# Optimization experiments

Hardware: AMD Instinct MI355X
Metric: run time of the kernel (lower is better)

## Reference

```python
import jax, jax.numpy as jnp
import numpy as np

N_CLASS, N_SUPPORT, N_QUERY = 5, 5, 15
C, T, V = 128, 8, 25
LN_EPS = 1e-12


def setup_inputs() -> dict:
    key = jax.random.key(0)
    ks = jax.random.split(key, 6)
    n_tot = N_CLASS * (N_SUPPORT + N_QUERY)
    inp = jax.random.normal(ks[0], (n_tot, C, T, V), dtype=jnp.float32)
    # episode labels: 20 consecutive samples per class (arange // per_class)
    target = (jnp.arange(n_tot, dtype=jnp.int32) // (N_SUPPORT + N_QUERY)).astype(jnp.int32)
    s = 0.02
    p = lambda k: jax.random.normal(k, (C, C), dtype=jnp.float32) * s
    return {
        'input': inp,
        'Wq': p(ks[1]), 'bq': jnp.zeros((C,), jnp.float32),
        'Wk': p(ks[2]), 'bk': jnp.zeros((C,), jnp.float32),
        'Wv': p(ks[3]), 'bv': jnp.zeros((C,), jnp.float32),
        'Wo': p(ks[4]), 'bo': jnp.zeros((C,), jnp.float32),
        'ln_g': jnp.ones((C,), jnp.float32), 'ln_b': jnp.zeros((C,), jnp.float32),
        'target': target,
        'n_support': N_SUPPORT,
    }


def _layer_norm(x, g, b):
    mu = x.mean(-1, keepdims=True)
    var = ((x - mu) ** 2).mean(-1, keepdims=True)
    return (x - mu) * jax.lax.rsqrt(var + LN_EPS) * g + b


def _episode_forward(input, Wq, bq, Wk, bk, Wv, bv, Wo, bo, ln_g, ln_b, target, n_support):
    n_tot, c, t, v = input.shape
    m = N_CLASS
    per_class = n_tot // m
    n_query = per_class - n_support
    n = m * n_query

    # support/query split (stable argsort == torch.where per class for sorted labels)
    order = jnp.argsort(target).reshape(m, per_class)
    supp_idx = order[:, :n_support]                      # (m, h)
    qry_idx = order[:, n_support:].reshape(-1)           # (n,)
    z_proto = input[supp_idx]                            # (m, h, c, t, v)
    zq = input[qry_idx]                                  # (n, c, t, v)

    # ---- hal(): pairwise cross-attention over the vertex axis ----
    mh = m * n_support
    zq_p = jnp.transpose(zq, (0, 2, 3, 1))                                   # (n, t, v, c)
    zp_p = jnp.transpose(z_proto.reshape(mh, c, t, v), (0, 2, 3, 1))          # (mh, t, v, c)
    cat = jnp.concatenate([zq_p, zp_p], axis=0)                               # (n1, t, v, c)
    n1 = cat.shape[0]

    # Q from each of the n1 items, K/V from each of the mh prototypes.
    # Equivalent to the original expand->reshape pairing, without duplicating K/V.
    Q = cat @ Wq + bq                                                         # (n1, t, v, c)
    K = zp_p @ Wk + bk                                                        # (mh, t, v, c)
    Vv = zp_p @ Wv + bv                                                       # (mh, t, v, c)
    scale = 1.0 / jnp.sqrt(jnp.asarray(c, dtype=Q.dtype))
    scores = jnp.einsum('ntqc,mtkc->nmtqk', Q, K) * scale                     # (n1, mh, t, v, v)
    attn = jax.nn.softmax(scores, axis=-1)
    ctx = jnp.einsum('nmtqk,mtkc->nmtqc', attn, Vv)                           # (n1, mh, t, v, c)
    out = _layer_norm(ctx @ Wo + bo + cat[:, None], ln_g, ln_b)               # residual + LN
    att = out.mean(axis=1)                                                    # (n1, t, v, c) mean over mh pairs

    zq_att = jnp.transpose(att[:n], (0, 3, 1, 2))                             # (n, c, t, v)
    proto_att = att[n:].reshape(m, n_support, t, v, c).mean(axis=1)           # (m, t, v, c)
    proto_att = jnp.transpose(proto_att, (0, 3, 1, 2))                        # (m, c, t, v)

    # ---- squared-Euclidean metric on flattened features ----
    zq_f = zq_att.reshape(n, -1)
    zp_f = proto_att.reshape(m, -1)
    dist = jnp.sum((zq_f[:, None, :] - zp_f[None, :, :]) ** 2, axis=-1)       # (n, m)

    log_p_y = jax.nn.log_softmax(-dist, axis=1).reshape(m, n_query, m)
    cls = jnp.arange(m)
    loss = -log_p_y[cls[:, None], jnp.arange(n_query)[None, :], cls[:, None]].mean()
    y_hat = jnp.argmax(log_p_y, axis=2)
    acc = (y_hat == cls[:, None]).astype(jnp.float32).mean()
    return loss, acc


def reference(input, Wq, bq, Wk, bk, Wv, bv, Wo, bo, ln_g, ln_b, target, n_support):
    return _episode_forward(input, Wq, bq, Wk, bk, Wv, bv, Wo, bo, ln_g, ln_b, target, n_support)
```

## Files before the change

kernel.cpp:

```cpp
#include <hip/hip_runtime.h>
#include <math.h>

#define NTOT 100
#define NQ   75
#define NP   25
#define CC   128
#define TT   8
#define VV   25
#define NCLS 5
#define NSUP 5
#define NQRY 15
#define ROW  (TT*VV*CC)
#define TILE (VV*CC)
#define ROWS_Q 20000
#define ROWS_S 5000
#define RB_Q 625
#define RB_S 157

typedef __attribute__((ext_vector_type(8))) short short8;
typedef __attribute__((ext_vector_type(16))) float f32x16;

typedef union { uint4 u4; short8 s8; } pk_t;

__device__ __forceinline__ ushort f2bf(float f) {
    uint u = __float_as_uint(f);
    u += 0x7FFFu + ((u >> 16) & 1u);
    return (ushort)(u >> 16);
}
__device__ __forceinline__ float bf2f(uint u16v) {
    return __uint_as_float(u16v << 16);
}
__device__ __forceinline__ uint pkbf(float a, float b) {
    return (uint)f2bf(a) | ((uint)f2bf(b) << 16);
}

__global__ __launch_bounds__(256) void k_prep(
    const float* __restrict__ input, const int* __restrict__ target,
    const float* __restrict__ Wq, const float* __restrict__ Wk,
    const float* __restrict__ Wv, const float* __restrict__ Wo,
    ushort* __restrict__ catQbf, ushort* __restrict__ catSbf,
    ushort* __restrict__ Wfrag, ushort* __restrict__ catC,
    int* __restrict__ counter) {
    __shared__ float smp[100 * 129];
    __shared__ int targ[NTOT];
    __shared__ int order[NTOT];
    int b = blockIdx.x, tid = threadIdx.x;

    if (b < 200) {
        int n = b >> 1, hf = b & 1;
        if (tid < NTOT) targ[tid] = target[tid];
        __syncthreads();
        if (tid < NTOT) {
            int ti = targ[tid], rank = 0;
            for (int j = 0; j < NTOT; ++j) {
                int tj = targ[j];
                rank += (tj < ti) || (tj == ti && j < tid);
            }
            order[rank] = tid;
        }
        __syncthreads();
        int src;
        if (n < NQ) { int m = n / NQRY, qq = n - m * NQRY; src = order[m * 20 + NSUP + qq]; }
        else        { int i = n - NQ; int m = i / NSUP, s = i - m * NSUP; src = order[m * 20 + s]; }

        const float* in = input + (size_t)src * ROW + hf * 100;
        for (int idx = tid; idx < 12800; idx += 256) {
            int c = idx / 100, tt = idx - c * 100;
            smp[tt * 129 + c] = in[c * 200 + tt];
        }
        __syncthreads();
        uint* cc = (uint*)catC + ((size_t)n * 200 + hf * 100) * 64;
        for (int e2 = tid; e2 < 6400; e2 += 256) {
            int r = e2 >> 6, c2 = e2 & 63;
            cc[r * 64 + c2] = pkbf(smp[r * 129 + c2 * 2], smp[r * 129 + c2 * 2 + 1]);
        }
        bool isSup = (n >= NQ);
        for (int o = tid; o < 1600; o += 256) {
            int k8 = o / 100, tt = o - k8 * 100;
            int base = tt * 129 + k8 * 8;
            uint4 pk;
            pk.x = pkbf(smp[base+0], smp[base+1]);
            pk.y = pkbf(smp[base+2], smp[base+3]);
            pk.z = pkbf(smp[base+4], smp[base+5]);
            pk.w = pkbf(smp[base+6], smp[base+7]);
            int row = n * 200 + hf * 100 + tt;
            size_t dst = (((size_t)(row >> 5) * 8 + (k8 >> 1)) * 64 + ((row & 31) + 32 * (k8 & 1))) * 8;
            *(uint4*)(catQbf + dst) = pk;
            if (isSup) {
                int r2 = (n - NQ) * 200 + hf * 100 + tt;
                size_t dst2 = (((size_t)(r2 >> 5) * 8 + (k8 >> 1)) * 64 + ((r2 & 31) + 32 * (k8 & 1))) * 8;
                *(uint4*)(catSbf + dst2) = pk;
            }
        }
    } else {
        int wi = b - 200;
        const float* W = (wi == 0) ? Wq : (wi == 1) ? Wk : (wi == 2) ? Wv : Wo;
        ushort* dstW = Wfrag + (size_t)wi * 16384;
        for (int o = tid; o < 2048; o += 256) {
            int k8 = o >> 7, c = o & 127;
            uint4 pk;
            pk.x = pkbf(W[(k8*8+0)*128 + c], W[(k8*8+1)*128 + c]);
            pk.y = pkbf(W[(k8*8+2)*128 + c], W[(k8*8+3)*128 + c]);
            pk.z = pkbf(W[(k8*8+4)*128 + c], W[(k8*8+5)*128 + c]);
            pk.w = pkbf(W[(k8*8+6)*128 + c], W[(k8*8+7)*128 + c]);
            size_t dst = ((size_t)((c >> 5) * 8 + (k8 >> 1)) * 64 + ((c & 31) + 32 * (k8 & 1))) * 8;
            *(uint4*)(dstW + dst) = pk;
        }
        if (wi == 3) {
            uint4 z = make_uint4(0, 0, 0, 0);
            for (int o = tid; o < 512; o += 256) {
                int ks = o >> 6, l = o & 63;
                if ((l & 31) >= 8)
                    *(uint4*)(catSbf + (((size_t)156 * 8 + ks) * 64 + l) * 8) = z;
            }
            if (tid == 0) *counter = 0;
        }
    }
}

__global__ __launch_bounds__(256) void k_proj(
    const ushort* __restrict__ catQbf, const ushort* __restrict__ catSbf,
    const ushort* __restrict__ Wfrag, const float* __restrict__ bq,
    const float* __restrict__ bk, const float* __restrict__ bv,
    ushort* __restrict__ Qf, ushort* __restrict__ Kf, ushort* __restrict__ Vf) {
    __shared__ ushort Vt[128 * 136];
    int b = blockIdx.x, tid = threadIdx.x;
    int w = tid >> 6, lane = tid & 63;
    int typ, rb0, nrb;
    if (b < 157)      { typ = 0; rb0 = b * 4;         nrb = RB_Q; }
    else if (b < 197) { typ = 1; rb0 = (b - 157) * 4; nrb = RB_S; }
    else              { typ = 2; rb0 = (b - 197) * 4; nrb = RB_S; }
    int rowblk = rb0 + w;
    bool act = rowblk < nrb;
    const ushort* src = (typ == 0) ? catQbf : catSbf;
    const ushort* Wf = Wfrag + (size_t)typ * 16384;
    const float* bias = (typ == 0) ? bq : (typ == 1) ? bk : bv;
    int rlimit = (typ == 0) ? ROWS_Q : ROWS_S;

    short8 af[8];
    if (act) {
        const ushort* ap = src + (size_t)rowblk * 4096 + lane * 8;
        #pragma unroll
        for (int ks = 0; ks < 8; ++ks) af[ks] = *(const short8*)(ap + ks * 512);
    }
    #pragma unroll
    for (int ct = 0; ct < 4; ++ct) {
        f32x16 Cm;
        #pragma unroll
        for (int r = 0; r < 16; ++r) Cm[r] = 0.f;
        if (act) {
            const ushort* bp = Wf + (size_t)(ct * 8) * 512 + lane * 8;
            #pragma unroll
            for (int ks = 0; ks < 8; ++ks) {
                short8 bf_ = *(const short8*)(bp + ks * 512);
                Cm = __builtin_amdgcn_mfma_f32_32x32x16_bf16(af[ks], bf_, Cm, 0, 0, 0);
            }
            float bcol = bias[ct * 32 + (lane & 31)];
            if (typ <= 1) {
                ushort* dstB = (typ == 0) ? Qf : Kf;
                #pragma unroll
                for (int r = 0; r < 16; ++r) {
                    int row = rowblk * 32 + (r & 3) + 8 * (r >> 2) + 4 * (lane >> 5);
                    if (row < rlimit) {
                        int c = ct * 32 + (lane & 31);
                        int st = row / 25, vv = row - st * 25;
                        size_t dst = (((size_t)st * 8 + (c >> 4)) * 64 + (vv + 32 * ((c >> 3) & 1))) * 8 + (c & 7);
                        dstB[dst] = f2bf(Cm[r] + bcol);
                    }
                }
            } else {
                #pragma unroll
                for (int r = 0; r < 16; ++r) {
                    int lrow = w * 32 + (r & 3) + 8 * (r >> 2) + 4 * (lane >> 5);
                    Vt[lrow * 136 + ct * 32 + (lane & 31)] = f2bf(Cm[r] + bcol);
                }
            }
        }
    }
    if (typ == 2) {
        __syncthreads();
        const ushort* WoF = Wfrag + (size_t)3 * 16384;
        short8 a2[8];
        if (act) {
            #pragma unroll
            for (int ks = 0; ks < 8; ++ks)
                a2[ks] = *(const short8*)(Vt + (w * 32 + (lane & 31)) * 136 + ks * 16 + (lane >> 5) * 8);
        }
        #pragma unroll
        for (int ct = 0; ct < 4; ++ct) {
            if (act) {
                f32x16 Cm;
                #pragma unroll
                for (int r = 0; r < 16; ++r) Cm[r] = 0.f;
                const ushort* bp = WoF + (size_t)(ct * 8) * 512 + lane * 8;
                #pragma unroll
                for (int ks = 0; ks < 8; ++ks) {
                    short8 bf_ = *(const short8*)(bp + ks * 512);
                    Cm = __builtin_amdgcn_mfma_f32_32x32x16_bf16(a2[ks], bf_, Cm, 0, 0, 0);
                }
                #pragma unroll
                for (int r = 0; r < 16; ++r) {
                    int row = rowblk * 32 + (r & 3) + 8 * (r >> 2) + 4 * (lane >> 5);
                    if (row < ROWS_S) {
                        int c = ct * 32 + (lane & 31);
                        int tile = row / 25, vv = row - tile * 25;
                        size_t dst = ((((size_t)tile * 4 + ct) * 2 + (vv >> 4)) * 64
                                      + ((c & 31) + 32 * ((vv & 15) >> 3))) * 8 + (vv & 7);
                        Vf[dst] = f2bf(Cm[r]);
                    }
                }
            }
        }
    }
}

__global__ __launch_bounds__(256, 2) void k_attn(
    const ushort* __restrict__ Qf, const ushort* __restrict__ Kf,
    const ushort* __restrict__ Vf, const ushort* __restrict__ catC,
    const float* __restrict__ bo, float* __restrict__ att) {
    __shared__ float catb[25 * 129];
    __shared__ float red[2][50][65];
    __shared__ ushort qls[4096];

    int pair = blockIdx.x;
    int t = pair & 7;
    int tid = threadIdx.x;
    int wv = tid >> 6, lane = tid & 63;
    int q = lane & 31, half = lane >> 5;

    {
        const uint* cc = (const uint*)catC + (size_t)pair * 1600;
        for (int i2 = tid; i2 < 1600; i2 += 256) {
            uint u = cc[i2];
            int r = i2 >> 6, c2 = (i2 & 63) * 2;
            catb[r * 129 + c2]     = bf2f(u & 0xffffu) + bo[c2];
            catb[r * 129 + c2 + 1] = bf2f(u >> 16) + bo[c2 + 1];
        }
    }
    {
        const uint* qp = (const uint*)(Qf + (size_t)pair * 4096);
        uint* ql = (uint*)qls;
        for (int i2 = tid; i2 < 2048; i2 += 256) ql[i2] = qp[i2];
    }
    __syncthreads();

    int qc = q < 25 ? q : 24;
    float attsum[64];
    #pragma unroll
    for (int i = 0; i < 64; ++i) attsum[i] = 0.f;
    float Csc = 0.f;

    const float CEXP = (float)(1.4426950408889634 * 0.08838834764831845);

    const ushort* kbase = Kf + (size_t)t * 4096 + lane * 8;
    short8 kf[8];
    #pragma unroll
    for (int ks = 0; ks < 8; ++ks)
        kf[ks] = *(const short8*)(kbase + (size_t)wv * 32768 + ks * 512);

    int cnt = (wv == 0) ? 7 : 6;
    for (int mi = 0; mi < cnt; ++mi) {
        int m = wv + 4 * mi;

        f32x16 S;
        #pragma unroll
        for (int r = 0; r < 16; ++r) S[r] = 0.f;
        #pragma unroll
        for (int ks = 0; ks < 8; ++ks) {
            short8 qv = *(const short8*)(qls + ks * 512 + lane * 8);
            S = __builtin_amdgcn_mfma_f32_32x32x16_bf16(kf[ks], qv, S, 0, 0, 0);
        }

        float p[16], mx = -3e38f;
        #pragma unroll
        for (int r = 0; r < 16; ++r) {
            int key = (r & 3) + 8 * (r >> 2) + 4 * half;
            float v = (key < 25) ? S[r] : -3e38f;
            p[r] = v; mx = fmaxf(mx, v);
        }
        mx = fmaxf(mx, __shfl_xor(mx, 32));
        float sum = 0.f;
        #pragma unroll
        for (int r = 0; r < 16; ++r) { p[r] = exp2f((p[r] - mx) * CEXP); sum += p[r]; }
        sum += __shfl_xor(sum, 32);
        float inv = 1.f / sum;

        const ushort* vp = Vf + ((size_t)(m * 8 + t)) * 4096 + lane * 8;
        short8 vf0 = *(const short8*)(vp);
        short8 vf1 = *(const short8*)(vp + 512);
        short8 vf2 = *(const short8*)(vp + 1024);
        short8 vf3 = *(const short8*)(vp + 1536);
        short8 vf4 = *(const short8*)(vp + 2048);
        short8 vf5 = *(const short8*)(vp + 2560);
        short8 vf6 = *(const short8*)(vp + 3072);
        short8 vf7 = *(const short8*)(vp + 3584);
        #pragma unroll
        for (int ks = 0; ks < 8; ++ks)
            kf[ks] = *(const short8*)(kbase + (size_t)(m + 4) * 32768 + ks * 512);

        uint o01   = pkbf(p[0] * inv,  p[1] * inv);
        uint o23   = pkbf(p[2] * inv,  p[3] * inv);
        uint o45   = pkbf(p[4] * inv,  p[5] * inv);
        uint o67   = pkbf(p[6] * inv,  p[7] * inv);
        uint o89   = pkbf(p[8] * inv,  p[9] * inv);
        uint o1011 = pkbf(p[10] * inv, p[11] * inv);
        uint o1213 = pkbf(p[12] * inv, p[13] * inv);
        uint o1415 = pkbf(p[14] * inv, p[15] * inv);
        bool h0 = (half == 0);
        uint rA = __shfl_xor(h0 ? o45 : o01, 32);
        uint rB = __shfl_xor(h0 ? o67 : o23, 32);
        uint rC = __shfl_xor(h0 ? o1213 : o89, 32);
        uint rD = __shfl_xor(h0 ? o1415 : o1011, 32);
        pk_t P0, P1;
        P0.u4 = h0 ? make_uint4(o01, o23, rA, rB) : make_uint4(rA, rB, o45, o67);
        P1.u4 = h0 ? make_uint4(o89, o1011, rC, rD) : make_uint4(rC, rD, o1213, o1415);
        short8 pb0 = P0.s8, pb1 = P1.s8;

        f32x16 ctx[4];
        #pragma unroll
        for (int mt = 0; mt < 4; ++mt) {
            #pragma unroll
            for (int r = 0; r < 16; ++r) ctx[mt][r] = 0.f;
        }
        ctx[0] = __builtin_amdgcn_mfma_f32_32x32x16_bf16(vf0, pb0, ctx[0], 0, 0, 0);
        ctx[0] = __builtin_amdgcn_mfma_f32_32x32x16_bf16(vf1, pb1, ctx[0], 0, 0, 0);
        ctx[1] = __builtin_amdgcn_mfma_f32_32x32x16_bf16(vf2, pb0, ctx[1], 0, 0, 0);
        ctx[1] = __builtin_amdgcn_mfma_f32_32x32x16_bf16(vf3, pb1, ctx[1], 0, 0, 0);
        ctx[2] = __builtin_amdgcn_mfma_f32_32x32x16_bf16(vf4, pb0, ctx[2], 0, 0, 0);
        ctx[2] = __builtin_amdgcn_mfma_f32_32x32x16_bf16(vf5, pb1, ctx[2], 0, 0, 0);
        ctx[3] = __builtin_amdgcn_mfma_f32_32x32x16_bf16(vf6, pb0, ctx[3], 0, 0, 0);
        ctx[3] = __builtin_amdgcn_mfma_f32_32x32x16_bf16(vf7, pb1, ctx[3], 0, 0, 0);

        float s1 = 0.f, s2 = 0.f;
        #pragma unroll
        for (int mt = 0; mt < 4; ++mt) {
            float t1 = 0.f, t2 = 0.f;
            #pragma unroll
            for (int r = 0; r < 16; ++r) {
                int c = mt * 32 + (r & 3) + 8 * (r >> 2) + 4 * half;
                float xv = ctx[mt][r] + catb[qc * 129 + c];
                ctx[mt][r] = xv;
                t1 += xv; t2 = fmaf(xv, xv, t2);
            }
            s1 += t1; s2 += t2;
        }
        s1 += __shfl_xor(s1, 32); s2 += __shfl_xor(s2, 32);
        float mu = s1 * (1.f / 128.f);
        float var = s2 * (1.f / 128.f) - mu * mu;
        var = fmaxf(var, 0.f);
        float rs = rsqrtf(var + 1e-12f);
        #pragma unroll
        for (int i = 0; i < 64; ++i)
            attsum[i] = fmaf(ctx[i >> 4][i & 15], rs, attsum[i]);
        Csc = fmaf(-mu, rs, Csc);
    }

    __syncthreads();
    int s = half * 25 + q;
    bool act = q < 25;
    if ((wv == 1 || wv == 3) && act) {
        float (*rg)[65] = red[wv >> 1];
        #pragma unroll
        for (int i = 0; i < 64; ++i) rg[s][i] = attsum[i];
        rg[s][64] = Csc;
    }
    __syncthreads();
    if ((wv == 0 || wv == 2) && act) {
        float (*rg)[65] = red[wv >> 1];
        #pragma unroll
        for (int i = 0; i < 64; ++i) attsum[i] += rg[s][i];
        Csc += rg[s][64];
    }
    __syncthreads();
    if (wv == 2 && act) {
        #pragma unroll
        for (int i = 0; i < 64; ++i) red[0][s][i] = attsum[i];
        red[0][s][64] = Csc;
    }
    __syncthreads();
    if (wv == 0 && act) {
        #pragma unroll
        for (int i = 0; i < 64; ++i) attsum[i] += red[0][s][i];
        Csc += red[0][s][64];
        float* ap = att + (size_t)pair * TILE + q * 128;
        #pragma unroll
        for (int mt = 0; mt < 4; ++mt) {
            #pragma unroll
            for (int rg4 = 0; rg4 < 4; ++rg4) {
                int c0 = mt * 32 + 8 * rg4 + 4 * half;
                int i0 = mt * 16 + rg4 * 4;
                float4 o;
                o.x = attsum[i0 + 0] + Csc; o.y = attsum[i0 + 1] + Csc;
                o.z = attsum[i0 + 2] + Csc; o.w = attsum[i0 + 3] + Csc;
                *(float4*)&ap[c0] = o;
            }
        }
    }
}

__global__ __launch_bounds__(256) void k_dist_loss(
    const float* __restrict__ att, const float* __restrict__ ln_g,
    float* __restrict__ dist, int* __restrict__ counter,
    float* __restrict__ out) {
    int b = blockIdx.x;
    int i = b / 5, j = b - 5 * i;
    const float4* a  = (const float4*)(att + (size_t)i * ROW);
    const float4* s0 = (const float4*)(att + (size_t)(NQ + j * 5 + 0) * ROW);
    const float4* s1p = (const float4*)(att + (size_t)(NQ + j * 5 + 1) * ROW);
    const float4* s2p = (const float4*)(att + (size_t)(NQ + j * 5 + 2) * ROW);
    const float4* s3p = (const float4*)(att + (size_t)(NQ + j * 5 + 3) * ROW);
    const float4* s4p = (const float4*)(att + (size_t)(NQ + j * 5 + 4) * ROW);
    float d = 0.f;
    for (int e4 = threadIdx.x; e4 < 6400; e4 += 256) {
        float4 av = a[e4];
        float4 q0 = s0[e4], q1 = s1p[e4], q2 = s2p[e4], q3 = s3p[e4], q4 = s4p[e4];
        float4 g4 = *(const float4*)(ln_g + (e4 & 31) * 4);
        float px = 0.2f * (q0.x + q1.x + q2.x + q3.x + q4.x);
        float py = 0.2f * (q0.y + q1.y + q2.y + q3.y + q4.y);
        float pz = 0.2f * (q0.z + q1.z + q2.z + q3.z + q4.z);
        float pw = 0.2f * (q0.w + q1.w + q2.w + q3.w + q4.w);
        float dx = av.x - px, dy = av.y - py, dz = av.z - pz, dw = av.w - pw;
        d = fmaf(g4.x * g4.x, dx * dx, d);
        d = fmaf(g4.y * g4.y, dy * dy, d);
        d = fmaf(g4.z * g4.z, dz * dz, d);
        d = fmaf(g4.w * g4.w, dw * dw, d);
    }
    #pragma unroll
    for (int msk = 32; msk >= 1; msk >>= 1) d += __shfl_xor(d, msk);
    __shared__ float part[4];
    __shared__ int lastFlag;
    int lane = threadIdx.x & 63, wv = threadIdx.x >> 6;
    if (lane == 0) part[wv] = d;
    __syncthreads();
    if (threadIdx.x == 0) {
        float total = (part[0] + part[1] + part[2] + part[3]) * (1.f / 625.f);
        __hip_atomic_store(&dist[b], total, __ATOMIC_RELEASE, __HIP_MEMORY_SCOPE_AGENT);
        int tk = __hip_atomic_fetch_add(counter, 1, __ATOMIC_ACQ_REL, __HIP_MEMORY_SCOPE_AGENT);
        lastFlag = (tk == 374);
    }
    __syncthreads();
    if (!lastFlag) return;

    int iq = threadIdx.x;
    float li = 0.f, ok = 0.f;
    if (iq < NQ) {
        float dd[5];
        #pragma unroll
        for (int jj = 0; jj < 5; ++jj)
            dd[jj] = __hip_atomic_load(&dist[iq * 5 + jj], __ATOMIC_ACQUIRE, __HIP_MEMORY_SCOPE_AGENT);
        int cls = iq / NQRY;
        float mind = dd[0];
        int best = 0;
        #pragma unroll
        for (int jj = 1; jj < 5; ++jj) {
            if (dd[jj] < mind) mind = dd[jj];
            if (dd[jj] < dd[best]) best = jj;
        }
        float sume = 0.f;
        #pragma unroll
        for (int jj = 0; jj < 5; ++jj) sume += expf(mind - dd[jj]);
        float lse = logf(sume) - mind;
        li = dd[cls] + lse;
        ok = (best == cls) ? 1.f : 0.f;
    }
    #pragma unroll
    for (int msk = 32; msk >= 1; msk >>= 1) {
        li += __shfl_xor(li, msk);
        ok += __shfl_xor(ok, msk);
    }
    if (lane == 0) { part[wv] = li; part[wv + 2] = ok; }
    __syncthreads();
    if (threadIdx.x == 0) {
        out[0] = (part[0] + part[1]) / 75.f;
        out[1] = (part[2] + part[3]) / 75.f;
    }
}

extern "C" void kernel_launch(void* const* d_in, const int* in_sizes, int n_in,
                              void* d_out, int out_size, void* d_ws, size_t ws_size,
                              hipStream_t stream) {
    const float* input = (const float*)d_in[0];
    const float* Wq   = (const float*)d_in[1];
    const float* bq   = (const float*)d_in[2];
    const float* Wk   = (const float*)d_in[3];
    const float* bk   = (const float*)d_in[4];
    const float* Wv   = (const float*)d_in[5];
    const float* bv   = (const float*)d_in[6];
    const float* Wo   = (const float*)d_in[7];
    const float* bo   = (const float*)d_in[8];
    const float* ln_g = (const float*)d_in[9];
    const float* ln_b = (const float*)d_in[10];
    const int* target = (const int*)d_in[11];
    float* out = (float*)d_out;
    (void)ln_b;

    float* ws = (float*)d_ws;
    ushort* catQbf = (ushort*)ws;
    ushort* catSbf = catQbf + (size_t)RB_Q * 4096;
    ushort* Wfrag  = catSbf + (size_t)RB_S * 4096;
    ushort* catC   = Wfrag + 65536;
    ushort* Qf     = catC + 2560000;
    ushort* Kf     = Qf + 3276800;
    ushort* Vf     = Kf + 819200;
    float*  att    = (float*)(Vf + 819200);
    float*  distb  = att + 2560000;
    int*    counter= (int*)(distb + 512);

    k_prep<<<204, 256, 0, stream>>>(input, target, Wq, Wk, Wv, Wo,
                                    catQbf, catSbf, Wfrag, catC, counter);
    k_proj<<<237, 256, 0, stream>>>(catQbf, catSbf, Wfrag, bq, bk, bv, Qf, Kf, Vf);
    k_attn<<<800, 256, 0, stream>>>(Qf, Kf, Vf, catC, bo, att);
    k_dist_loss<<<375, 256, 0, stream>>>(att, ln_g, distb, counter, out);
}
```

Before: 186.5 us.

## Fuse prep into projection kernel, loading input directly into MFMA fragments

Removes the separate prep kernel. The projection kernel now gathers input rows straight from global memory into bf16 MFMA A-fragments, builds the weight fragments in LDS, and writes catC from registers. Each block handling support rows computes K, then V, then the Wo projection in sequence. This drops one launch and the catQbf/catSbf/Wfrag round-trips through global memory. In exchange, the input loads are strided by 200 floats per lane (poorly coalesced), every block redundantly recomputes the sort ranks and re-converts the weights, and the support blocks run longer serial chains.

```diff
diff --git a/kernel.cpp b/kernel.cpp
--- a/kernel.cpp
+++ b/kernel.cpp
@@ -34,184 +34,202 @@
     return (uint)f2bf(a) | ((uint)f2bf(b) << 16);
 }
 
-__global__ __launch_bounds__(256) void k_prep(
+__global__ __launch_bounds__(256) void k_proj(
     const float* __restrict__ input, const int* __restrict__ target,
     const float* __restrict__ Wq, const float* __restrict__ Wk,
     const float* __restrict__ Wv, const float* __restrict__ Wo,
-    ushort* __restrict__ catQbf, ushort* __restrict__ catSbf,
-    ushort* __restrict__ Wfrag, ushort* __restrict__ catC,
+    const float* __restrict__ bq, const float* __restrict__ bk,
+    const float* __restrict__ bv,
+    ushort* __restrict__ catC, ushort* __restrict__ Qf,
+    ushort* __restrict__ Kf, ushort* __restrict__ Vf,
     int* __restrict__ counter) {
-    __shared__ float smp[100 * 129];
-    __shared__ int targ[NTOT];
-    __shared__ int order[NTOT];
+    __shared__ ushort WfragLDS[16384];
+    __shared__ ushort VtFrag[16384];
+
     int b = blockIdx.x, tid = threadIdx.x;
-
-    if (b < 200) {
-        int n = b >> 1, hf = b & 1;
-        if (tid < NTOT) targ[tid] = target[tid];
+    int w = tid >> 6, lane = tid & 63, half = lane >> 5, l31 = lane & 31;
+
+    if (b == 0 && tid == 0) *counter = 0;
+
+    int* iscr = (int*)VtFrag;
+    if (tid < NTOT) iscr[tid] = target[tid];
+    __syncthreads();
+    if (tid < NTOT) {
+        int ti = iscr[tid], rank = 0;
+        for (int j = 0; j < NTOT; ++j) {
+            int tj = iscr[j];
+            rank += (tj < ti) || (tj == ti && j < tid);
+        }
+        iscr[128 + rank] = tid;
+    }
+    __syncthreads();
+
+    bool isQ = b < 157;
+    int rowblk = isQ ? (b * 4 + w) : ((b - 157) * 4 + w);
+    int nrb = isQ ? RB_Q : RB_S;
+    bool act = rowblk < nrb;
+    int rlimit = isQ ? ROWS_Q : ROWS_S;
+    int grow = rowblk * 32 + l31;
+    int growc = grow < rlimit ? grow : rlimit - 1;
+    int n = growc / 200;
+    int tv = growc - n * 200;
+    int src;
+    {
+        int nn = isQ ? n : (NQ + n);
+        if (nn < NQ) { int m = nn / NQRY, qq = nn - m * NQRY; src = iscr[128 + m * 20 + NSUP + qq]; }
+        else         { int i2 = nn - NQ; int m = i2 / NSUP, s = i2 - m * NSUP; src = iscr[128 + m * 20 + s]; }
+    }
+    __syncthreads();
+
+    const float* inp = input + (size_t)src * ROW + tv;
+    short8 af[8];
+    #pragma unroll
+    for (int ks = 0; ks < 8; ++ks) {
+        float f0 = inp[(ks * 16 + half * 8 + 0) * 200];
+        float f1 = inp[(ks * 16 + half * 8 + 1) * 200];
+        float f2 = inp[(ks * 16 + half * 8 + 2) * 200];
+        float f3 = inp[(ks * 16 + half * 8 + 3) * 200];
+        float f4 = inp[(ks * 16 + half * 8 + 4) * 200];
+        float f5 = inp[(ks * 16 + half * 8 + 5) * 200];
+        float f6 = inp[(ks * 16 + half * 8 + 6) * 200];
+        float f7 = inp[(ks * 16 + half * 8 + 7) * 200];
+        pk_t u;
+        u.u4 = make_uint4(pkbf(f0, f1), pkbf(f2, f3), pkbf(f4, f5), pkbf(f6, f7));
+        af[ks] = u.s8;
+    }
+
+    #define BUILDW(W) do {                                                       \
+        for (int o = tid; o < 2048; o += 256) {                                  \
+            int k8 = o >> 7, c = o & 127;                                        \
+            uint4 pk;                                                            \
+            pk.x = pkbf((W)[(k8*8+0)*128 + c], (W)[(k8*8+1)*128 + c]);           \
+            pk.y = pkbf((W)[(k8*8+2)*128 + c], (W)[(k8*8+3)*128 + c]);           \
+            pk.z = pkbf((W)[(k8*8+4)*128 + c], (W)[(k8*8+5)*128 + c]);           \
+            pk.w = pkbf((W)[(k8*8+6)*128 + c], (W)[(k8*8+7)*128 + c]);           \
+            int dst = (((c >> 5) * 8 + (k8 >> 1)) * 64 + ((c & 31) + 32 * (k8 & 1))) * 8; \
+            *(uint4*)(WfragLDS + dst) = pk;                                      \
+        }                                                                        \
+    } while (0)
+
+    if (isQ) {
+        BUILDW(Wq);
         __syncthreads();
-        if (tid < NTOT) {
-            int ti = targ[tid], rank = 0;
-            for (int j = 0; j < NTOT; ++j) {
-                int tj = targ[j];
-                rank += (tj < ti) || (tj == ti && j < tid);
-            }
-            order[rank] = tid;
-        }
-        __syncthreads();
-        int src;
-        if (n < NQ) { int m = n / NQRY, qq = n - m * NQRY; src = order[m * 20 + NSUP + qq]; }
-        else        { int i = n - NQ; int m = i / NSUP, s = i - m * NSUP; src = order[m * 20 + s]; }
-
-        const float* in = input + (size_t)src * ROW + hf * 100;
-        for (int idx = tid; idx < 12800; idx += 256) {
-            int c = idx / 100, tt = idx - c * 100;
-            smp[tt * 129 + c] = in[c * 200 + tt];
-        }
-        __syncthreads();
-        uint* cc = (uint*)catC + ((size_t)n * 200 + hf * 100) * 64;
-        for (int e2 = tid; e2 < 6400; e2 += 256) {
-            int r = e2 >> 6, c2 = e2 & 63;
-            cc[r * 64 + c2] = pkbf(smp[r * 129 + c2 * 2], smp[r * 129 + c2 * 2 + 1]);
-        }
-        bool isSup = (n >= NQ);
-        for (int o = tid; o < 1600; o += 256) {
-            int k8 = o / 100, tt = o - k8 * 100;
-            int base = tt * 129 + k8 * 8;
-            uint4 pk;
-            pk.x = pkbf(smp[base+0], smp[base+1]);
-            pk.y = pkbf(smp[base+2], smp[base+3]);
-            pk.z = pkbf(smp[base+4], smp[base+5]);
-            pk.w = pkbf(smp[base+6], smp[base+7]);
-            int row = n * 200 + hf * 100 + tt;
-            size_t dst = (((size_t)(row >> 5) * 8 + (k8 >> 1)) * 64 + ((row & 31) + 32 * (k8 & 1))) * 8;
-            *(uint4*)(catQbf + dst) = pk;
-            if (isSup) {
-                int r2 = (n - NQ) * 200 + hf * 100 + tt;
-                size_t dst2 = (((size_t)(r2 >> 5) * 8 + (k8 >> 1)) * 64 + ((r2 & 31) + 32 * (k8 & 1))) * 8;
-                *(uint4*)(catSbf + dst2) = pk;
-            }
-        }
-    } else {
-        int wi = b - 200;
-        const float* W = (wi == 0) ? Wq : (wi == 1) ? Wk : (wi == 2) ? Wv : Wo;
-        ushort* dstW = Wfrag + (size_t)wi * 16384;
-        for (int o = tid; o < 2048; o += 256) {
-            int k8 = o >> 7, c = o & 127;
-            uint4 pk;
-            pk.x = pkbf(W[(k8*8+0)*128 + c], W[(k8*8+1)*128 + c]);
-            pk.y = pkbf(W[(k8*8+2)*128 + c], W[(k8*8+3)*128 + c]);
-            pk.z = pkbf(W[(k8*8+4)*128 + c], W[(k8*8+5)*128 + c]);
-            pk.w = pkbf(W[(k8*8+6)*128 + c], W[(k8*8+7)*128 + c]);
-            size_t dst = ((size_t)((c >> 5) * 8 + (k8 >> 1)) * 64 + ((c & 31) + 32 * (k8 & 1))) * 8;
-            *(uint4*)(dstW + dst) = pk;
-        }
-        if (wi == 3) {
-            uint4 z = make_uint4(0, 0, 0, 0);
-            for (int o = tid; o < 512; o += 256) {
-                int ks = o >> 6, l = o & 63;
-                if ((l & 31) >= 8)
-                    *(uint4*)(catSbf + (((size_t)156 * 8 + ks) * 64 + l) * 8) = z;
-            }
-            if (tid == 0) *counter = 0;
-        }
-    }
-}
-
-__global__ __launch_bounds__(256) void k_proj(
-    const ushort* __restrict__ catQbf, const ushort* __restrict__ catSbf,
-    const ushort* __restrict__ Wfrag, const float* __restrict__ bq,
-    const float* __restrict__ bk, const float* __restrict__ bv,
-    ushort* __restrict__ Qf, ushort* __restrict__ Kf, ushort* __restrict__ Vf) {
-    __shared__ ushort Vt[128 * 136];
-    int b = blockIdx.x, tid = threadIdx.x;
-    int w = tid >> 6, lane = tid & 63;
-    int typ, rb0, nrb;
-    if (b < 157)      { typ = 0; rb0 = b * 4;         nrb = RB_Q; }
-    else if (b < 197) { typ = 1; rb0 = (b - 157) * 4; nrb = RB_S; }
-    else              { typ = 2; rb0 = (b - 197) * 4; nrb = RB_S; }
-    int rowblk = rb0 + w;
-    bool act = rowblk < nrb;
-    const ushort* src = (typ == 0) ? catQbf : catSbf;
-    const ushort* Wf = Wfrag + (size_t)typ * 16384;
-    const float* bias = (typ == 0) ? bq : (typ == 1) ? bk : bv;
-    int rlimit = (typ == 0) ? ROWS_Q : ROWS_S;
-
-    short8 af[8];
-    if (act) {
-        const ushort* ap = src + (size_t)rowblk * 4096 + lane * 8;
-        #pragma unroll
-        for (int ks = 0; ks < 8; ++ks) af[ks] = *(const short8*)(ap + ks * 512);
-    }
-    #pragma unroll
-    for (int ct = 0; ct < 4; ++ct) {
-        f32x16 Cm;
-        #pragma unroll
-        for (int r = 0; r < 16; ++r) Cm[r] = 0.f;
-        if (act) {
-            const ushort* bp = Wf + (size_t)(ct * 8) * 512 + lane * 8;
+        #pragma unroll
+        for (int ct = 0; ct < 4; ++ct) {
+            if (!act) continue;
+            f32x16 Cm;
+            #pragma unroll
+            for (int r = 0; r < 16; ++r) Cm[r] = 0.f;
+            const ushort* bp = WfragLDS + ct * 8 * 512 + lane * 8;
             #pragma unroll
             for (int ks = 0; ks < 8; ++ks) {
                 short8 bf_ = *(const short8*)(bp + ks * 512);
                 Cm = __builtin_amdgcn_mfma_f32_32x32x16_bf16(af[ks], bf_, Cm, 0, 0, 0);
             }
-            float bcol = bias[ct * 32 + (lane & 31)];
-            if (typ <= 1) {
-                ushort* dstB = (typ == 0) ? Qf : Kf;
-                #pragma unroll
-                for (int r = 0; r < 16; ++r) {
-                    int row = rowblk * 32 + (r & 3) + 8 * (r >> 2) + 4 * (lane >> 5);
-                    if (row < rlimit) {
-                        int c = ct * 32 + (lane & 31);
-                        int st = row / 25, vv = row - st * 25;
-                        size_t dst = (((size_t)st * 8 + (c >> 4)) * 64 + (vv + 32 * ((c >> 3) & 1))) * 8 + (c & 7);
-                        dstB[dst] = f2bf(Cm[r] + bcol);
-                    }
+            float bcol = bq[ct * 32 + l31];
+            #pragma unroll
+            for (int r = 0; r < 16; ++r) {
+                int row = rowblk * 32 + (r & 3) + 8 * (r >> 2) + 4 * half;
+                if (row < ROWS_Q) {
+                    int c = ct * 32 + l31;
+                    int st = row / 25, vv = row - st * 25;
+                    size_t dst = (((size_t)st * 8 + (c >> 4)) * 64 + (vv + 32 * ((c >> 3) & 1))) * 8 + (c & 7);
+                    Qf[dst] = f2bf(Cm[r] + bcol);
                 }
-            } else {
-                #pragma unroll
-                for (int r = 0; r < 16; ++r) {
-                    int lrow = w * 32 + (r & 3) + 8 * (r >> 2) + 4 * (lane >> 5);
-                    Vt[lrow * 136 + ct * 32 + (lane & 31)] = f2bf(Cm[r] + bcol);
+            }
+        }
+        if (act) {
+            ushort* cc = catC + (size_t)grow * 128 + half * 8;
+            #pragma unroll
+            for (int ks = 0; ks < 8; ++ks)
+                *(short8*)(cc + ks * 16) = af[ks];
+        }
+    } else {
+        BUILDW(Wk);
+        __syncthreads();
+        #pragma unroll
+        for (int ct = 0; ct < 4; ++ct) {
+            if (!act) continue;
+            f32x16 Cm;
+            #pragma unroll
+            for (int r = 0; r < 16; ++r) Cm[r] = 0.f;
+            const ushort* bp = WfragLDS + ct * 8 * 512 + lane * 8;
+            #pragma unroll
+            for (int ks = 0; ks < 8; ++ks) {
+                short8 bf_ = *(const short8*)(bp + ks * 512);
+                Cm = __builtin_amdgcn_mfma_f32_32x32x16_bf16(af[ks], bf_, Cm, 0, 0, 0);
+            }
+            float bcol = bk[ct * 32 + l31];
+            #pragma unroll
+            for (int r = 0; r < 16; ++r) {
+                int row = rowblk * 32 + (r & 3) + 8 * (r >> 2) + 4 * half;
+                if (row < ROWS_S) {
+                    int c = ct * 32 + l31;
+                    int st = row / 25, vv = row - st * 25;
+                    size_t dst = (((size_t)st * 8 + (c >> 4)) * 64 + (vv + 32 * ((c >> 3) & 1))) * 8 + (c & 7);
+                    Kf[dst] = f2bf(Cm[r] + bcol);
                 }
             }
         }
-    }
-    if (typ == 2) {
         __syncthreads();
-        const ushort* WoF = Wfrag + (size_t)3 * 16384;
+        BUILDW(Wv);
+        __syncthreads();
+        #pragma unroll
+        for (int ct = 0; ct < 4; ++ct) {
+            if (!act) continue;
+            f32x16 Cm;
+            #pragma unroll
+            for (int r = 0; r < 16; ++r) Cm[r] = 0.f;
+            const ushort* bp = WfragLDS + ct * 8 * 512 + lane * 8;
+            #pragma unroll
+            for (int ks = 0; ks < 8; ++ks) {
+                short8 bf_ = *(const short8*)(bp + ks * 512);
+                Cm = __builtin_amdgcn_mfma_f32_32x32x16_bf16(af[ks], bf_, Cm, 0, 0, 0);
+            }
+            float bcol = bv[ct * 32 + l31];
+            int c = ct * 32 + l31;
+            int ks2 = c >> 4, lh = (c >> 3) & 1, j2 = c & 7;
+            #pragma unroll
+            for (int r = 0; r < 16; ++r) {
+                int rowLocal = (r & 3) + 8 * (r >> 2) + 4 * half;
+                VtFrag[w * 4096 + ks2 * 512 + (rowLocal + 32 * lh) * 8 + j2] = f2bf(Cm[r] + bcol);
+            }
+        }
+        __syncthreads();
+        BUILDW(Wo);
+        __syncthreads();
         short8 a2[8];
         if (act) {
             #pragma unroll
             for (int ks = 0; ks < 8; ++ks)
-                a2[ks] = *(const short8*)(Vt + (w * 32 + (lane & 31)) * 136 + ks * 16 + (lane >> 5) * 8);
+                a2[ks] = *(const short8*)(VtFrag + w * 4096 + ks * 512 + lane * 8);
         }
         #pragma unroll
         for (int ct = 0; ct < 4; ++ct) {
-            if (act) {
-                f32x16 Cm;
-                #pragma unroll
-                for (int r = 0; r < 16; ++r) Cm[r] = 0.f;
-                const ushort* bp = WoF + (size_t)(ct * 8) * 512 + lane * 8;
-                #pragma unroll
-                for (int ks = 0; ks < 8; ++ks) {
-                    short8 bf_ = *(const short8*)(bp + ks * 512);
-                    Cm = __builtin_amdgcn_mfma_f32_32x32x16_bf16(a2[ks], bf_, Cm, 0, 0, 0);
+            if (!act) continue;
+            f32x16 Cm;
+            #pragma unroll
+            for (int r = 0; r < 16; ++r) Cm[r] = 0.f;
+            const ushort* bp = WfragLDS + ct * 8 * 512 + lane * 8;
+            #pragma unroll
+            for (int ks = 0; ks < 8; ++ks) {
+                short8 bf_ = *(const short8*)(bp + ks * 512);
+                Cm = __builtin_amdgcn_mfma_f32_32x32x16_bf16(a2[ks], bf_, Cm, 0, 0, 0);
+            }
+            #pragma unroll
+            for (int r = 0; r < 16; ++r) {
+                int row = rowblk * 32 + (r & 3) + 8 * (r >> 2) + 4 * half;
+                if (row < ROWS_S) {
+                    int c = ct * 32 + l31;
+                    int tile = row / 25, vv = row - tile * 25;
+                    size_t dst = ((((size_t)tile * 4 + ct) * 2 + (vv >> 4)) * 64
+                                  + ((c & 31) + 32 * ((vv & 15) >> 3))) * 8 + (vv & 7);
+                    Vf[dst] = f2bf(Cm[r]);
                 }
-                #pragma unroll
-                for (int r = 0; r < 16; ++r) {
-                    int row = rowblk * 32 + (r & 3) + 8 * (r >> 2) + 4 * (lane >> 5);
-                    if (row < ROWS_S) {
-                        int c = ct * 32 + (lane & 31);
-                        int tile = row / 25, vv = row - tile * 25;
-                        size_t dst = ((((size_t)tile * 4 + ct) * 2 + (vv >> 4)) * 64
-                                      + ((c & 31) + 32 * ((vv & 15) >> 3))) * 8 + (vv & 7);
-                        Vf[dst] = f2bf(Cm[r]);
-                    }
-                }
-            }
-        }
-    }
+            }
+        }
+    }
+    #undef BUILDW
 }
 
 __global__ __launch_bounds__(256, 2) void k_attn(
@@ -495,20 +513,16 @@
     (void)ln_b;
 
     float* ws = (float*)d_ws;
-    ushort* catQbf = (ushort*)ws;
-    ushort* catSbf = catQbf + (size_t)RB_Q * 4096;
-    ushort* Wfrag  = catSbf + (size_t)RB_S * 4096;
-    ushort* catC   = Wfrag + 65536;
-    ushort* Qf     = catC + 2560000;
-    ushort* Kf     = Qf + 3276800;
-    ushort* Vf     = Kf + 819200;
-    float*  att    = (float*)(Vf + 819200);
-    float*  distb  = att + 2560000;
-    int*    counter= (int*)(distb + 512);
-
-    k_prep<<<204, 256, 0, stream>>>(input, target, Wq, Wk, Wv, Wo,
-                                    catQbf, catSbf, Wfrag, catC, counter);
-    k_proj<<<237, 256, 0, stream>>>(catQbf, catSbf, Wfrag, bq, bk, bv, Qf, Kf, Vf);
+    ushort* catC = (ushort*)ws;
+    ushort* Qf   = catC + 2560000;
+    ushort* Kf   = Qf + 3276800;
+    ushort* Vf   = Kf + 819200;
+    float*  att  = (float*)(Vf + 819200);
+    float*  distb = att + 2560000;
+    int*    counter = (int*)(distb + 512);
+
+    k_proj<<<197, 256, 0, stream>>>(input, target, Wq, Wk, Wv, Wo, bq, bk, bv,
+                                    catC, Qf, Kf, Vf, counter);
     k_attn<<<800, 256, 0, stream>>>(Qf, Kf, Vf, catC, bo, att);
     k_dist_loss<<<375, 256, 0, stream>>>(att, ln_g, distb, counter, out);
 }
```

Result: no change. 187.1 us (+0.3%).
